# Kernel tuning notes

Measured on AMD Instinct MI355X. Metric: run time of the kernel, lower is better.

The kernel has to match this reference:

```python
import jax, jax.numpy as jnp
import numpy as np

B, L, H, N, O = 64, 512, 768, 50, 768
ALPHA = 0.3  # leaky relu slope in GAT
NEG_INF = -9e15


def _position_encoding(n, d):
    # standard sinusoidal PE, shape [n, d]
    pos = jnp.arange(n, dtype=jnp.float32)[:, None]              # [n,1]
    div = jnp.exp(jnp.arange(0, d, 2, dtype=jnp.float32) * (-np.log(10000.0) / d))  # [d/2]
    ang = pos * div[None, :]                                     # [n, d/2]
    return jnp.stack([jnp.sin(ang), jnp.cos(ang)], axis=-1).reshape(n, d)


def _gat_layer(x, adj, W, b, a, ab):
    # Dense GAT layer. Original builds an [N,N,2F] concat tensor then applies
    # linear a; mathematically identical to splitting a into src/dst halves.
    Wh = x @ W + b                                               # [N,F]
    Fdim = Wh.shape[-1]
    a_src = Wh @ a[:Fdim]                                        # [N]
    a_dst = Wh @ a[Fdim:]                                        # [N]
    e = jax.nn.leaky_relu(a_src[:, None] + a_dst[None, :] + ab, negative_slope=ALPHA)
    att = jax.nn.softmax(jnp.where(adj > 0, e, NEG_INF), axis=1)  # rows sum to 1
    return att @ Wh                                              # [N,F]


def setup_inputs() -> dict:
    key = jax.random.key(0)
    ks = jax.random.split(key, 16)
    s = 1.0 / np.sqrt(H)
    utter_embedding = jax.random.normal(ks[0], (B, L, H), jnp.float32)
    cls_ids = jnp.sort(jax.random.randint(ks[1], (B, N), 0, L), axis=1).astype(jnp.int32)
    adj = jax.random.randint(ks[2], (B, N, N), 0, 2).astype(jnp.int32)
    adj = adj | jnp.eye(N, dtype=jnp.int32)  # ensure self loops so softmax rows are valid
    return {
        "utter_embedding": utter_embedding,
        "cls_ids": cls_ids,
        "adj": adj,
        # GAT head 0 (concat=True)
        "W1": jax.random.normal(ks[3], (H, H), jnp.float32) * s,
        "b1": jnp.zeros((H,), jnp.float32),
        "a1": jax.random.normal(ks[4], (2 * H,), jnp.float32) * s,
        "ab1": jnp.zeros((), jnp.float32),
        # GAT out layer (concat=False)
        "W2": jax.random.normal(ks[5], (H, H), jnp.float32) * s,
        "b2": jnp.zeros((H,), jnp.float32),
        "a2": jax.random.normal(ks[6], (2 * H,), jnp.float32) * s,
        "ab2": jnp.zeros((), jnp.float32),
        # Attention pooling over utterances
        "Wa": jax.random.normal(ks[7], (H, H), jnp.float32) * s,
        "ba": jnp.zeros((H,), jnp.float32),
        "v": jax.random.normal(ks[8], (H,), jnp.float32) * s,
        # Final linear
        "Wl": jax.random.normal(ks[9], (H, O), jnp.float32) * s,
        "bl": jnp.zeros((O,), jnp.float32),
    }


def reference(utter_embedding, cls_ids, adj, W1, b1, a1, ab1, W2, b2, a2, ab2,
              Wa, ba, v, Wl, bl):
    pe = _position_encoding(N, H)                                # [N,H]

    def per_dialogue(emb, ids, A):
        # gather [CLS] utterance embeddings: index_select
        x = jnp.take(emb, ids, axis=0)                           # [N,H]
        x = x + pe                                               # position encoder
        # GAT: 1 head concat -> elu, out layer -> elu, residual
        h = jax.nn.elu(_gat_layer(x, A, W1, b1, a1, ab1))
        h = jax.nn.elu(_gat_layer(h, A, W2, b2, a2, ab2)) + x    # residual per GAT.forward
        # attention pooling over N utterances
        scores = jax.nn.softmax(jnp.tanh(h @ Wa + ba) @ v, axis=0)  # [N]
        return scores @ h                                        # [H]

    dialogue = jax.vmap(per_dialogue)(utter_embedding, cls_ids, adj)  # [B,H]
    return dialogue @ Wl + bl                                    # [B,O]
```

## Files before the change

kernel.cpp:

```cpp
#include <hip/hip_runtime.h>
#include <hip/hip_bf16.h>
#include <math.h>

typedef __attribute__((ext_vector_type(8))) short bf16x8;
typedef __attribute__((ext_vector_type(4))) float f32x4;
typedef __attribute__((ext_vector_type(4))) unsigned short u16x4;

constexpr int Bn = 64;
constexpr int Ln = 512;
constexpr int Hd = 768;
constexpr int Nn = 50;
constexpr int On = 768;
constexpr int RP = 64;

__device__ __forceinline__ f32x4 MFMA(bf16x8 a, bf16x8 b, f32x4 c) {
  return __builtin_amdgcn_mfma_f32_16x16x32_bf16(a, b, c, 0, 0, 0);
}
__device__ __forceinline__ unsigned short f2bb(float v) {
  __hip_bfloat16 h = __float2bfloat16(v);
  return *(unsigned short*)&h;
}

struct PrepArgs {
  const float* src[4];
  __hip_bfloat16* dst[4];
  const float* emb;
  const int* ids;
  float* xres;
  __hip_bfloat16* xb;
  float* aux;
};

__global__ __launch_bounds__(256) void prep_kernel(PrepArgs a) {
  int bx = blockIdx.x;
  if (bx < 2304) {
    __shared__ float tile[32][33];
    int job = bx / 576, t = bx % 576;
    const float* W = a.src[job];
    __hip_bfloat16* Wt = a.dst[job];
    int tx = (t % 24) * 32, ty = (t / 24) * 32;
    int c = threadIdx.x & 31, r0 = threadIdx.x >> 5;
    for (int r = r0; r < 32; r += 8)
      tile[r][c] = W[(size_t)(tx + r) * Hd + ty + c];
    __syncthreads();
    for (int r = r0; r < 32; r += 8)
      Wt[(size_t)(ty + r) * Hd + tx + c] = __float2bfloat16(tile[c][r]);
  } else if (bx < 6400) {
    int bn = bx - 2304;
    int b = bn >> 6, i = bn & 63;
    __hip_bfloat16* xbo = a.xb + (size_t)bn * Hd;
    float* xro = a.xres + (size_t)bn * Hd;
    if (i < Nn) {
      int id = a.ids[b * Nn + i];
      const float* src = a.emb + ((size_t)b * Ln + id) * Hd;
      const float kLog = 9.210340371976184f / (float)Hd;
      for (int h = threadIdx.x; h < Hd; h += 256) {
        float freq = expf(-(float)(h & ~1) * kLog);
        float ang = (float)i * freq;
        float v = src[h] + ((h & 1) ? cosf(ang) : sinf(ang));
        xbo[h] = __float2bfloat16(v);
        xro[h] = v;
      }
    } else {
      for (int h = threadIdx.x; h < Hd; h += 256) {
        xbo[h] = __float2bfloat16(0.f);
        xro[h] = 0.f;
      }
    }
  } else {
    int idx = (bx - 6400) * 256 + threadIdx.x;
    if (idx < 5 * Bn * RP) a.aux[idx] = 0.f;
  }
}

template <int EPI>
__global__ __launch_bounds__(256) void gemm_kernel(
    const __hip_bfloat16* __restrict__ A, const __hip_bfloat16* __restrict__ Bt,
    const float* __restrict__ bias, __hip_bfloat16* __restrict__ WhT,
    const float* __restrict__ avec, float* __restrict__ o1,
    float* __restrict__ o2) {
  __shared__ __hip_bfloat16 As[2][64][40];
  __shared__ __hip_bfloat16 Bs[2][64][40];
  int tid = threadIdx.x;
  int wave = tid >> 6, lane = tid & 63;
  int lr = lane & 15, lq = lane >> 4;
  int b = blockIdx.x, col0 = blockIdx.y * 64;
  int row0 = b * RP;
  int sr = tid >> 2, sk = (tid & 3) * 8;
  const __hip_bfloat16* Ap = A + (size_t)(row0 + sr) * Hd + sk;
  const __hip_bfloat16* Bp = Bt + (size_t)(col0 + sr) * Hd + sk;
  uint4 ra = *(const uint4*)Ap;
  uint4 rb = *(const uint4*)Bp;
  *(uint4*)&As[0][sr][sk] = ra;
  *(uint4*)&Bs[0][sr][sk] = rb;
  f32x4 acc[4] = {};
  __syncthreads();
  int cur = 0;
  for (int kt = 32; kt < Hd; kt += 32) {
    ra = *(const uint4*)(Ap + kt);
    rb = *(const uint4*)(Bp + kt);
    bf16x8 af = *(const bf16x8*)&As[cur][wave * 16 + lr][lq * 8];
#pragma unroll
    for (int ct = 0; ct < 4; ++ct)
      acc[ct] = MFMA(af, *(const bf16x8*)&Bs[cur][ct * 16 + lr][lq * 8], acc[ct]);
    *(uint4*)&As[cur ^ 1][sr][sk] = ra;
    *(uint4*)&Bs[cur ^ 1][sr][sk] = rb;
    __syncthreads();
    cur ^= 1;
  }
  {
    bf16x8 af = *(const bf16x8*)&As[cur][wave * 16 + lr][lq * 8];
#pragma unroll
    for (int ct = 0; ct < 4; ++ct)
      acc[ct] = MFMA(af, *(const bf16x8*)&Bs[cur][ct * 16 + lr][lq * 8], acc[ct]);
  }
  int lrow0 = wave * 16 + lq * 4;
  if (EPI == 0) {
    float ps[4] = {}, pd[4] = {};
#pragma unroll
    for (int ct = 0; ct < 4; ++ct) {
      int gc = col0 + ct * 16 + lr;
      float bv = bias[gc];
      float a_s = avec[gc], a_d = avec[Hd + gc];
      u16x4 pk;
#pragma unroll
      for (int r = 0; r < 4; ++r) {
        float v = acc[ct][r] + bv;
        pk[r] = f2bb(v);
        ps[r] += v * a_s;
        pd[r] += v * a_d;
      }
      *(u16x4*)(WhT + ((size_t)b * Hd + gc) * RP + lrow0) = pk;
    }
#pragma unroll
    for (int off = 8; off; off >>= 1)
#pragma unroll
      for (int r = 0; r < 4; ++r) {
        ps[r] += __shfl_xor(ps[r], off);
        pd[r] += __shfl_xor(pd[r], off);
      }
    if (lr == 0)
#pragma unroll
      for (int r = 0; r < 4; ++r) {
        int row = lrow0 + r;
        if (row < Nn) {
          atomicAdd(&o1[b * RP + row], ps[r]);
          atomicAdd(&o2[b * RP + row], pd[r]);
        }
      }
  } else {
    float pr[4] = {};
#pragma unroll
    for (int ct = 0; ct < 4; ++ct) {
      int gc = col0 + ct * 16 + lr;
      float bv = bias[gc];
      float vv_ = avec[gc];
#pragma unroll
      for (int r = 0; r < 4; ++r) pr[r] += tanhf(acc[ct][r] + bv) * vv_;
    }
#pragma unroll
    for (int off = 8; off; off >>= 1)
#pragma unroll
      for (int r = 0; r < 4; ++r) pr[r] += __shfl_xor(pr[r], off);
    if (lr == 0)
#pragma unroll
      for (int r = 0; r < 4; ++r) {
        int row = lrow0 + r;
        if (row < Nn) atomicAdd(&o1[b * RP + row], pr[r]);
      }
  }
}

template <int LAYER>
__global__ __launch_bounds__(256) void attf_kernel(
    const float* __restrict__ ssrc, const float* __restrict__ sdst,
    const int* __restrict__ adj, const float* __restrict__ ab,
    const __hip_bfloat16* __restrict__ WhT, const float* __restrict__ xres,
    float* __restrict__ hf, __hip_bfloat16* __restrict__ hb) {
  int b = blockIdx.x / 3, cg = blockIdx.x % 3;
  __shared__ float attL[Nn * 52];
  __shared__ __hip_bfloat16 attB[64 * 72];
  int tid = threadIdx.x;
  float abv = ab[0];
  for (int i = tid; i < 64 * 72; i += 256) attB[i] = __float2bfloat16(0.f);
  for (int idx = tid; idx < Nn * Nn; idx += 256) {
    int i = idx / Nn, j = idx - i * Nn;
    float t = ssrc[b * RP + i] + sdst[b * RP + j] + abv;
    t = t > 0.f ? t : 0.3f * t;
    attL[i * 52 + j] = (adj[(size_t)b * Nn * Nn + idx] > 0) ? t : -9.0e15f;
  }
  __syncthreads();
  if (tid < Nn) {
    float m = -3.0e38f;
    for (int j = 0; j < Nn; ++j) m = fmaxf(m, attL[tid * 52 + j]);
    float s = 0.f;
    for (int j = 0; j < Nn; ++j) {
      float p = expf(attL[tid * 52 + j] - m);
      attL[tid * 52 + j] = p;
      s += p;
    }
    float inv = 1.f / s;
    for (int j = 0; j < Nn; ++j) attL[tid * 52 + j] *= inv;
  }
  __syncthreads();
  for (int idx = tid; idx < Nn * Nn; idx += 256) {
    int i = idx / Nn, j = idx - i * Nn;
    attB[i * 72 + j] = __float2bfloat16(attL[i * 52 + j]);
  }
  __syncthreads();

  int w = tid >> 6, lane = tid & 63, lr = lane & 15, lq = lane >> 4;
  bf16x8 a0 = *(const bf16x8*)&attB[(w * 16 + lr) * 72 + lq * 8];
  bf16x8 a1 = *(const bf16x8*)&attB[(w * 16 + lr) * 72 + 32 + lq * 8];
#pragma unroll
  for (int s = 0; s < 16; ++s) {
    int gc = cg * 256 + s * 16 + lr;
    const __hip_bfloat16* Bp = WhT + ((size_t)b * Hd + gc) * RP + lq * 8;
    f32x4 acc = {};
    acc = MFMA(a0, *(const bf16x8*)Bp, acc);
    acc = MFMA(a1, *(const bf16x8*)(Bp + 32), acc);
#pragma unroll
    for (int r = 0; r < 4; ++r) {
      float v = acc[r];
      v = v > 0.f ? v : expf(v) - 1.f;
      size_t off = ((size_t)b * RP + w * 16 + lq * 4 + r) * Hd + gc;
      if (LAYER == 2) {
        v += xres[off];
        hf[off] = v;
      }
      hb[off] = __float2bfloat16(v);
    }
  }
}

__global__ __launch_bounds__(256) void poolfinal_kernel(
    const float* __restrict__ sraw, const float* __restrict__ h2,
    const __hip_bfloat16* __restrict__ Wlt, const float* __restrict__ bl,
    float* __restrict__ out) {
  int b = blockIdx.x;
  __shared__ float sc[Nn];
  __shared__ float ds[Hd];
  if (threadIdx.x < 64) {
    int j = threadIdx.x;
    float e = (j < Nn) ? sraw[b * RP + j] : -3.0e38f;
    float m = e;
#pragma unroll
    for (int off = 32; off; off >>= 1) m = fmaxf(m, __shfl_xor(m, off));
    float p = (j < Nn) ? expf(e - m) : 0.f;
    float s = p;
#pragma unroll
    for (int off = 32; off; off >>= 1) s += __shfl_xor(s, off);
    if (j < Nn) sc[j] = p / s;
  }
  __syncthreads();
  for (int h = threadIdx.x; h < Hd; h += 256) {
    float a = 0.f;
#pragma unroll 10
    for (int j = 0; j < Nn; ++j) a += sc[j] * h2[((size_t)b * RP + j) * Hd + h];
    ds[h] = a;
  }
  __syncthreads();
  for (int oo = 0; oo < 3; ++oo) {
    int o = oo * 256 + threadIdx.x;
    float acc = bl[o];
    const uint4* wr = (const uint4*)(Wlt + (size_t)o * Hd);
    for (int kk = 0; kk < Hd / 8; ++kk) {
      union { uint4 u; unsigned short s[8]; } w;
      w.u = wr[kk];
#pragma unroll
      for (int t = 0; t < 8; ++t)
        acc += ds[kk * 8 + t] * __uint_as_float((unsigned)w.s[t] << 16);
    }
    out[(size_t)b * On + o] = acc;
  }
}

extern "C" void kernel_launch(void* const* d_in, const int* in_sizes, int n_in,
                              void* d_out, int out_size, void* d_ws, size_t ws_size,
                              hipStream_t stream) {
  const float* emb = (const float*)d_in[0];
  const int* ids = (const int*)d_in[1];
  const int* adj = (const int*)d_in[2];
  const float* W1 = (const float*)d_in[3];
  const float* b1 = (const float*)d_in[4];
  const float* a1 = (const float*)d_in[5];
  const float* ab1 = (const float*)d_in[6];
  const float* W2 = (const float*)d_in[7];
  const float* b2 = (const float*)d_in[8];
  const float* a2 = (const float*)d_in[9];
  const float* ab2 = (const float*)d_in[10];
  const float* Wa = (const float*)d_in[11];
  const float* ba = (const float*)d_in[12];
  const float* vv = (const float*)d_in[13];
  const float* Wl = (const float*)d_in[14];
  const float* bl = (const float*)d_in[15];
  float* out = (float*)d_out;

  char* p = (char*)d_ws;
  auto alloc = [&](size_t bytes) {
    char* r = p;
    p += (bytes + 255) & ~(size_t)255;
    return r;
  };
  __hip_bfloat16* Wt1 = (__hip_bfloat16*)alloc((size_t)Hd * Hd * 2);
  __hip_bfloat16* Wt2 = (__hip_bfloat16*)alloc((size_t)Hd * Hd * 2);
  __hip_bfloat16* Wta = (__hip_bfloat16*)alloc((size_t)Hd * Hd * 2);
  __hip_bfloat16* Wlt = (__hip_bfloat16*)alloc((size_t)Hd * On * 2);
  float* aux = (float*)alloc((size_t)5 * Bn * RP * 4);
  float* ssrc1 = aux;
  float* sdst1 = aux + Bn * RP;
  float* ssrc2 = aux + 2 * Bn * RP;
  float* sdst2 = aux + 3 * Bn * RP;
  float* sraw = aux + 4 * Bn * RP;
  __hip_bfloat16* xb = (__hip_bfloat16*)alloc((size_t)Bn * RP * Hd * 2);
  float* xres = (float*)alloc((size_t)Bn * RP * Hd * 4);
  __hip_bfloat16* WhT1 = (__hip_bfloat16*)alloc((size_t)Bn * Hd * RP * 2);
  __hip_bfloat16* WhT2 = (__hip_bfloat16*)alloc((size_t)Bn * Hd * RP * 2);
  __hip_bfloat16* h1b = (__hip_bfloat16*)alloc((size_t)Bn * RP * Hd * 2);
  __hip_bfloat16* h2b = (__hip_bfloat16*)alloc((size_t)Bn * RP * Hd * 2);
  float* h2f = (float*)alloc((size_t)Bn * RP * Hd * 4);

  PrepArgs pa;
  pa.src[0] = W1; pa.src[1] = W2; pa.src[2] = Wa; pa.src[3] = Wl;
  pa.dst[0] = Wt1; pa.dst[1] = Wt2; pa.dst[2] = Wta; pa.dst[3] = Wlt;
  pa.emb = emb; pa.ids = ids; pa.xres = xres; pa.xb = xb; pa.aux = aux;
  prep_kernel<<<6480, 256, 0, stream>>>(pa);

  dim3 ggrid(Bn, Hd / 64);
  dim3 agrid(Bn * 3);

  gemm_kernel<0><<<ggrid, 256, 0, stream>>>(xb, Wt1, b1, WhT1, a1, ssrc1, sdst1);
  attf_kernel<1><<<agrid, 256, 0, stream>>>(ssrc1, sdst1, adj, ab1, WhT1,
                                            nullptr, nullptr, h1b);
  gemm_kernel<0><<<ggrid, 256, 0, stream>>>(h1b, Wt2, b2, WhT2, a2, ssrc2, sdst2);
  attf_kernel<2><<<agrid, 256, 0, stream>>>(ssrc2, sdst2, adj, ab2, WhT2, xres,
                                            h2f, h2b);
  gemm_kernel<1><<<ggrid, 256, 0, stream>>>(h2b, Wta, ba, nullptr, vv, sraw,
                                            nullptr);
  poolfinal_kernel<<<Bn, 256, 0, stream>>>(sraw, h2f, Wlt, bl, out);
}
```

Baseline: 302.9 us.

## Fuse GAT pipeline into persistent megakernel with per-dialogue dependency counters

Six separate launches (three GEMMs, two attention kernels, pooling) are replaced by one persistent kernel of 512 blocks. Work moves between stages through per-dialogue atomic counters that blocks spin on, so dialogues can advance without whole-grid barriers. This removes launch gaps and tail effects between stages. In exchange it relies on all 512 blocks being co-resident (two per CU) to avoid deadlock, and it adds spin-wait and fence overhead.

```diff
diff --git a/kernel.cpp b/kernel.cpp
--- a/kernel.cpp
+++ b/kernel.cpp
@@ -12,6 +12,9 @@
 constexpr int Nn = 50;
 constexpr int On = 768;
 constexpr int RP = 64;
+
+constexpr int NCNT = 5 * Bn;
+constexpr int AUXW = 5 * Bn * RP + NCNT;
 
 __device__ __forceinline__ f32x4 MFMA(bf16x8 a, bf16x8 b, f32x4 c) {
   return __builtin_amdgcn_mfma_f32_16x16x32_bf16(a, b, c, 0, 0, 0);
@@ -69,22 +72,42 @@
     }
   } else {
     int idx = (bx - 6400) * 256 + threadIdx.x;
-    if (idx < 5 * Bn * RP) a.aux[idx] = 0.f;
-  }
-}
+    if (idx < AUXW) a.aux[idx] = 0.f;
+  }
+}
+
+__device__ __forceinline__ void wait_cnt(const int* c, int need) {
+  if (threadIdx.x == 0) {
+    while (__hip_atomic_load(c, __ATOMIC_ACQUIRE, __HIP_MEMORY_SCOPE_AGENT) <
+           need) {
+      __builtin_amdgcn_s_sleep(2);
+    }
+  }
+  __syncthreads();
+}
+__device__ __forceinline__ void signal_cnt(int* c) {
+  __syncthreads();
+  if (threadIdx.x == 0) {
+    __threadfence();
+    __hip_atomic_fetch_add(c, 1, __ATOMIC_RELEASE, __HIP_MEMORY_SCOPE_AGENT);
+  }
+}
+
 
 template <int EPI>
-__global__ __launch_bounds__(256) void gemm_kernel(
-    const __hip_bfloat16* __restrict__ A, const __hip_bfloat16* __restrict__ Bt,
-    const float* __restrict__ bias, __hip_bfloat16* __restrict__ WhT,
-    const float* __restrict__ avec, float* __restrict__ o1,
-    float* __restrict__ o2) {
-  __shared__ __hip_bfloat16 As[2][64][40];
-  __shared__ __hip_bfloat16 Bs[2][64][40];
+__device__ void gemm_task(char* smemraw, int b, int col0,
+                          const __hip_bfloat16* __restrict__ A,
+                          const __hip_bfloat16* __restrict__ Bt,
+                          const float* __restrict__ bias,
+                          __hip_bfloat16* __restrict__ WhT,
+                          const float* __restrict__ avec,
+                          float* __restrict__ o1, float* __restrict__ o2) {
+  typedef __hip_bfloat16 Tile[64][40];
+  Tile* As = reinterpret_cast<Tile*>(smemraw);
+  Tile* Bs = reinterpret_cast<Tile*>(smemraw + 10240);
   int tid = threadIdx.x;
   int wave = tid >> 6, lane = tid & 63;
   int lr = lane & 15, lq = lane >> 4;
-  int b = blockIdx.x, col0 = blockIdx.y * 64;
   int row0 = b * RP;
   int sr = tid >> 2, sk = (tid & 3) * 8;
   const __hip_bfloat16* Ap = A + (size_t)(row0 + sr) * Hd + sk;
@@ -172,14 +195,18 @@
 }
 
 template <int LAYER>
-__global__ __launch_bounds__(256) void attf_kernel(
-    const float* __restrict__ ssrc, const float* __restrict__ sdst,
-    const int* __restrict__ adj, const float* __restrict__ ab,
-    const __hip_bfloat16* __restrict__ WhT, const float* __restrict__ xres,
-    float* __restrict__ hf, __hip_bfloat16* __restrict__ hb) {
-  int b = blockIdx.x / 3, cg = blockIdx.x % 3;
-  __shared__ float attL[Nn * 52];
-  __shared__ __hip_bfloat16 attB[64 * 72];
+__device__ void attf_task(char* smemraw, int b, int cg,
+                          const float* __restrict__ ssrc,
+                          const float* __restrict__ sdst,
+                          const int* __restrict__ adj,
+                          const float* __restrict__ ab,
+                          const __hip_bfloat16* __restrict__ WhT,
+                          const float* __restrict__ xres,
+                          float* __restrict__ hf,
+                          __hip_bfloat16* __restrict__ hb) {
+  float* attL = reinterpret_cast<float*>(smemraw);
+  __hip_bfloat16* attB =
+      reinterpret_cast<__hip_bfloat16*>(smemraw + Nn * 52 * 4);
   int tid = threadIdx.x;
   float abv = ab[0];
   for (int i = tid; i < 64 * 72; i += 256) attB[i] = __float2bfloat16(0.f);
@@ -233,13 +260,13 @@
   }
 }
 
-__global__ __launch_bounds__(256) void poolfinal_kernel(
-    const float* __restrict__ sraw, const float* __restrict__ h2,
-    const __hip_bfloat16* __restrict__ Wlt, const float* __restrict__ bl,
-    float* __restrict__ out) {
-  int b = blockIdx.x;
-  __shared__ float sc[Nn];
-  __shared__ float ds[Hd];
+__device__ void pool_task(char* smemraw, int b, const float* __restrict__ sraw,
+                          const float* __restrict__ h2,
+                          const __hip_bfloat16* __restrict__ Wlt,
+                          const float* __restrict__ bl,
+                          float* __restrict__ out) {
+  float* sc = reinterpret_cast<float*>(smemraw);
+  float* ds = reinterpret_cast<float*>(smemraw + 256);
   if (threadIdx.x < 64) {
     int j = threadIdx.x;
     float e = (j < Nn) ? sraw[b * RP + j] : -3.0e38f;
@@ -272,6 +299,68 @@
         acc += ds[kk * 8 + t] * __uint_as_float((unsigned)w.s[t] << 16);
     }
     out[(size_t)b * On + o] = acc;
+  }
+}
+
+struct MegaArgs {
+  const __hip_bfloat16 *xb, *Wt1, *Wt2, *Wta, *Wlt;
+  const float *xres;
+  const float *b1, *a1, *ab1, *b2, *a2, *ab2, *ba, *vv, *bl;
+  const int* adj;
+  float *ssrc1, *sdst1, *ssrc2, *sdst2, *sraw;
+  __hip_bfloat16 *WhT1, *WhT2, *h1b, *h2b;
+  float *h2f;
+  float* out;
+  int* cnt;
+};
+
+__global__ __launch_bounds__(256, 2) void mega_kernel(MegaArgs m) {
+  __shared__ __align__(16) char smem[20608];
+  int g = blockIdx.x;
+  int* c1 = m.cnt;
+  int* c2 = c1 + Bn;
+  int* c3 = c2 + Bn;
+  int* c4 = c3 + Bn;
+  int* c5 = c4 + Bn;
+
+  for (int t = g; t < 768; t += 512) {
+    int b = t / 12;
+    gemm_task<0>(smem, b, (t % 12) * 64, m.xb, m.Wt1, m.b1, m.WhT1, m.a1,
+                 m.ssrc1, m.sdst1);
+    signal_cnt(&c1[b]);
+  }
+  if (g >= 256 && g < 448) {
+    int t = g - 256, b = t / 3;
+    wait_cnt(&c1[b], 12);
+    attf_task<1>(smem, b, t % 3, m.ssrc1, m.sdst1, m.adj, m.ab1, m.WhT1,
+                 nullptr, nullptr, m.h1b);
+    signal_cnt(&c2[b]);
+  }
+  for (int t = g; t < 768; t += 512) {
+    int b = t / 12;
+    wait_cnt(&c2[b], 3);
+    gemm_task<0>(smem, b, (t % 12) * 64, m.h1b, m.Wt2, m.b2, m.WhT2, m.a2,
+                 m.ssrc2, m.sdst2);
+    signal_cnt(&c3[b]);
+  }
+  if (g >= 320) {
+    int t = 511 - g, b = t / 3;
+    wait_cnt(&c3[b], 12);
+    attf_task<2>(smem, b, t % 3, m.ssrc2, m.sdst2, m.adj, m.ab2, m.WhT2,
+                 m.xres, m.h2f, m.h2b);
+    signal_cnt(&c4[b]);
+  }
+  for (int t = g; t < 768; t += 512) {
+    int b = t / 12;
+    wait_cnt(&c4[b], 3);
+    gemm_task<1>(smem, b, (t % 12) * 64, m.h2b, m.Wta, m.ba, nullptr, m.vv,
+                 m.sraw, nullptr);
+    signal_cnt(&c5[b]);
+  }
+  if (g >= 448) {
+    int b = g - 448;
+    wait_cnt(&c5[b], 12);
+    pool_task(smem, b, m.sraw, m.h2f, m.Wlt, m.bl, m.out);
   }
 }
 
@@ -306,12 +395,13 @@
   __hip_bfloat16* Wt2 = (__hip_bfloat16*)alloc((size_t)Hd * Hd * 2);
   __hip_bfloat16* Wta = (__hip_bfloat16*)alloc((size_t)Hd * Hd * 2);
   __hip_bfloat16* Wlt = (__hip_bfloat16*)alloc((size_t)Hd * On * 2);
-  float* aux = (float*)alloc((size_t)5 * Bn * RP * 4);
+  float* aux = (float*)alloc((size_t)AUXW * 4);
   float* ssrc1 = aux;
   float* sdst1 = aux + Bn * RP;
   float* ssrc2 = aux + 2 * Bn * RP;
   float* sdst2 = aux + 3 * Bn * RP;
   float* sraw = aux + 4 * Bn * RP;
+  int* cnt = (int*)(aux + 5 * Bn * RP);
   __hip_bfloat16* xb = (__hip_bfloat16*)alloc((size_t)Bn * RP * Hd * 2);
   float* xres = (float*)alloc((size_t)Bn * RP * Hd * 4);
   __hip_bfloat16* WhT1 = (__hip_bfloat16*)alloc((size_t)Bn * Hd * RP * 2);
@@ -324,18 +414,18 @@
   pa.src[0] = W1; pa.src[1] = W2; pa.src[2] = Wa; pa.src[3] = Wl;
   pa.dst[0] = Wt1; pa.dst[1] = Wt2; pa.dst[2] = Wta; pa.dst[3] = Wlt;
   pa.emb = emb; pa.ids = ids; pa.xres = xres; pa.xb = xb; pa.aux = aux;
-  prep_kernel<<<6480, 256, 0, stream>>>(pa);
-
-  dim3 ggrid(Bn, Hd / 64);
-  dim3 agrid(Bn * 3);
-
-  gemm_kernel<0><<<ggrid, 256, 0, stream>>>(xb, Wt1, b1, WhT1, a1, ssrc1, sdst1);
-  attf_kernel<1><<<agrid, 256, 0, stream>>>(ssrc1, sdst1, adj, ab1, WhT1,
-                                            nullptr, nullptr, h1b);
-  gemm_kernel<0><<<ggrid, 256, 0, stream>>>(h1b, Wt2, b2, WhT2, a2, ssrc2, sdst2);
-  attf_kernel<2><<<agrid, 256, 0, stream>>>(ssrc2, sdst2, adj, ab2, WhT2, xres,
-                                            h2f, h2b);
-  gemm_kernel<1><<<ggrid, 256, 0, stream>>>(h2b, Wta, ba, nullptr, vv, sraw,
-                                            nullptr);
-  poolfinal_kernel<<<Bn, 256, 0, stream>>>(sraw, h2f, Wlt, bl, out);
-}
+  prep_kernel<<<6482, 256, 0, stream>>>(pa);
+
+  MegaArgs ma;
+  ma.xb = xb; ma.Wt1 = Wt1; ma.Wt2 = Wt2; ma.Wta = Wta; ma.Wlt = Wlt;
+  ma.xres = xres;
+  ma.b1 = b1; ma.a1 = a1; ma.ab1 = ab1;
+  ma.b2 = b2; ma.a2 = a2; ma.ab2 = ab2;
+  ma.ba = ba; ma.vv = vv; ma.bl = bl;
+  ma.adj = adj;
+  ma.ssrc1 = ssrc1; ma.sdst1 = sdst1; ma.ssrc2 = ssrc2; ma.sdst2 = sdst2;
+  ma.sraw = sraw;
+  ma.WhT1 = WhT1; ma.WhT2 = WhT2; ma.h1b = h1b; ma.h2b = h2b;
+  ma.h2f = h2f; ma.out = out; ma.cnt = cnt;
+  mega_kernel<<<512, 256, 0, stream>>>(ma);
+}
```

After: 604.1 us. +99.5%, slower.

## Deepen GEMM K-tile to 64 and split attention and pooling across more blocks

Applied to the files above, without the earlier changes.

The GEMM kernel now stages 64-wide K slices per iteration instead of 32, halving the number of barrier and global-load rounds per tile. The attention kernel splits each dialogue's output columns over 12 blocks instead of 3, and the pooling/final kernel over 3 blocks, so more CUs get work. The cost is that attention softmax and the pooling reduction are recomputed redundantly in every split block, and LDS use in the GEMM grows.

```diff
diff --git a/kernel.cpp b/kernel.cpp
--- a/kernel.cpp
+++ b/kernel.cpp
@@ -79,8 +79,8 @@
     const float* __restrict__ bias, __hip_bfloat16* __restrict__ WhT,
     const float* __restrict__ avec, float* __restrict__ o1,
     float* __restrict__ o2) {
-  __shared__ __hip_bfloat16 As[2][64][40];
-  __shared__ __hip_bfloat16 Bs[2][64][40];
+  __shared__ __hip_bfloat16 As[2][64][72];
+  __shared__ __hip_bfloat16 Bs[2][64][72];
   int tid = threadIdx.x;
   int wave = tid >> 6, lane = tid & 63;
   int lr = lane & 15, lq = lane >> 4;
@@ -89,30 +89,44 @@
   int sr = tid >> 2, sk = (tid & 3) * 8;
   const __hip_bfloat16* Ap = A + (size_t)(row0 + sr) * Hd + sk;
   const __hip_bfloat16* Bp = Bt + (size_t)(col0 + sr) * Hd + sk;
-  uint4 ra = *(const uint4*)Ap;
-  uint4 rb = *(const uint4*)Bp;
-  *(uint4*)&As[0][sr][sk] = ra;
-  *(uint4*)&Bs[0][sr][sk] = rb;
+  uint4 ra0 = *(const uint4*)Ap;
+  uint4 ra1 = *(const uint4*)(Ap + 32);
+  uint4 rb0 = *(const uint4*)Bp;
+  uint4 rb1 = *(const uint4*)(Bp + 32);
+  *(uint4*)&As[0][sr][sk] = ra0;
+  *(uint4*)&As[0][sr][sk + 32] = ra1;
+  *(uint4*)&Bs[0][sr][sk] = rb0;
+  *(uint4*)&Bs[0][sr][sk + 32] = rb1;
   f32x4 acc[4] = {};
   __syncthreads();
   int cur = 0;
-  for (int kt = 32; kt < Hd; kt += 32) {
-    ra = *(const uint4*)(Ap + kt);
-    rb = *(const uint4*)(Bp + kt);
-    bf16x8 af = *(const bf16x8*)&As[cur][wave * 16 + lr][lq * 8];
-#pragma unroll
-    for (int ct = 0; ct < 4; ++ct)
-      acc[ct] = MFMA(af, *(const bf16x8*)&Bs[cur][ct * 16 + lr][lq * 8], acc[ct]);
-    *(uint4*)&As[cur ^ 1][sr][sk] = ra;
-    *(uint4*)&Bs[cur ^ 1][sr][sk] = rb;
+  for (int kt = 64; kt < Hd; kt += 64) {
+    ra0 = *(const uint4*)(Ap + kt);
+    ra1 = *(const uint4*)(Ap + kt + 32);
+    rb0 = *(const uint4*)(Bp + kt);
+    rb1 = *(const uint4*)(Bp + kt + 32);
+    bf16x8 af0 = *(const bf16x8*)&As[cur][wave * 16 + lr][lq * 8];
+    bf16x8 af1 = *(const bf16x8*)&As[cur][wave * 16 + lr][32 + lq * 8];
+#pragma unroll
+    for (int ct = 0; ct < 4; ++ct) {
+      acc[ct] = MFMA(af0, *(const bf16x8*)&Bs[cur][ct * 16 + lr][lq * 8], acc[ct]);
+      acc[ct] = MFMA(af1, *(const bf16x8*)&Bs[cur][ct * 16 + lr][32 + lq * 8], acc[ct]);
+    }
+    *(uint4*)&As[cur ^ 1][sr][sk] = ra0;
+    *(uint4*)&As[cur ^ 1][sr][sk + 32] = ra1;
+    *(uint4*)&Bs[cur ^ 1][sr][sk] = rb0;
+    *(uint4*)&Bs[cur ^ 1][sr][sk + 32] = rb1;
     __syncthreads();
     cur ^= 1;
   }
   {
-    bf16x8 af = *(const bf16x8*)&As[cur][wave * 16 + lr][lq * 8];
-#pragma unroll
-    for (int ct = 0; ct < 4; ++ct)
-      acc[ct] = MFMA(af, *(const bf16x8*)&Bs[cur][ct * 16 + lr][lq * 8], acc[ct]);
+    bf16x8 af0 = *(const bf16x8*)&As[cur][wave * 16 + lr][lq * 8];
+    bf16x8 af1 = *(const bf16x8*)&As[cur][wave * 16 + lr][32 + lq * 8];
+#pragma unroll
+    for (int ct = 0; ct < 4; ++ct) {
+      acc[ct] = MFMA(af0, *(const bf16x8*)&Bs[cur][ct * 16 + lr][lq * 8], acc[ct]);
+      acc[ct] = MFMA(af1, *(const bf16x8*)&Bs[cur][ct * 16 + lr][32 + lq * 8], acc[ct]);
+    }
   }
   int lrow0 = wave * 16 + lq * 4;
   if (EPI == 0) {
@@ -177,7 +191,7 @@
     const int* __restrict__ adj, const float* __restrict__ ab,
     const __hip_bfloat16* __restrict__ WhT, const float* __restrict__ xres,
     float* __restrict__ hf, __hip_bfloat16* __restrict__ hb) {
-  int b = blockIdx.x / 3, cg = blockIdx.x % 3;
+  int b = blockIdx.x / 12, cg = blockIdx.x % 12;
   __shared__ float attL[Nn * 52];
   __shared__ __hip_bfloat16 attB[64 * 72];
   int tid = threadIdx.x;
@@ -213,8 +227,8 @@
   bf16x8 a0 = *(const bf16x8*)&attB[(w * 16 + lr) * 72 + lq * 8];
   bf16x8 a1 = *(const bf16x8*)&attB[(w * 16 + lr) * 72 + 32 + lq * 8];
 #pragma unroll
-  for (int s = 0; s < 16; ++s) {
-    int gc = cg * 256 + s * 16 + lr;
+  for (int s = 0; s < 4; ++s) {
+    int gc = cg * 64 + s * 16 + lr;
     const __hip_bfloat16* Bp = WhT + ((size_t)b * Hd + gc) * RP + lq * 8;
     f32x4 acc = {};
     acc = MFMA(a0, *(const bf16x8*)Bp, acc);
@@ -237,7 +251,7 @@
     const float* __restrict__ sraw, const float* __restrict__ h2,
     const __hip_bfloat16* __restrict__ Wlt, const float* __restrict__ bl,
     float* __restrict__ out) {
-  int b = blockIdx.x;
+  int b = blockIdx.x / 3, q = blockIdx.x % 3;
   __shared__ float sc[Nn];
   __shared__ float ds[Hd];
   if (threadIdx.x < 64) {
@@ -260,8 +274,8 @@
     ds[h] = a;
   }
   __syncthreads();
-  for (int oo = 0; oo < 3; ++oo) {
-    int o = oo * 256 + threadIdx.x;
+  {
+    int o = q * 256 + threadIdx.x;
     float acc = bl[o];
     const uint4* wr = (const uint4*)(Wlt + (size_t)o * Hd);
     for (int kk = 0; kk < Hd / 8; ++kk) {
@@ -327,7 +341,8 @@
   prep_kernel<<<6480, 256, 0, stream>>>(pa);
 
   dim3 ggrid(Bn, Hd / 64);
-  dim3 agrid(Bn * 3);
+  dim3 agrid(Bn * 12);
+  dim3 pgrid(Bn * 3);
 
   gemm_kernel<0><<<ggrid, 256, 0, stream>>>(xb, Wt1, b1, WhT1, a1, ssrc1, sdst1);
   attf_kernel<1><<<agrid, 256, 0, stream>>>(ssrc1, sdst1, adj, ab1, WhT1,
@@ -337,5 +352,5 @@
                                             h2f, h2b);
   gemm_kernel<1><<<ggrid, 256, 0, stream>>>(h2b, Wta, ba, nullptr, vv, sraw,
                                             nullptr);
-  poolfinal_kernel<<<Bn, 256, 0, stream>>>(sraw, h2f, Wlt, bl, out);
-}
+  poolfinal_kernel<<<pgrid, 256, 0, stream>>>(sraw, h2f, Wlt, bl, out);
+}
```

New measurement: 265.8 us. 12.2% less time.
